# Kernel tuning notes

Measured on AMD Instinct MI355X. Metric: run time of the kernel, lower is better.

The kernel has to match this reference:

```python
import jax, jax.numpy as jnp
import numpy as np

M = 8      # number of modalities (len(ModalityType))
D = 256    # embedding_dim
B = 8192   # batch size


def setup_inputs() -> dict:
    key = jax.random.key(0)
    ks = jax.random.split(key, 12)
    s = 1.0 / np.sqrt(D)
    x = jax.random.normal(ks[0], (M, B, D), dtype=jnp.float32)
    reasoning_query = jax.random.normal(ks[1], (B, D), dtype=jnp.float32)
    # Per ordered modality pair (src, tgt): seq_len=1 MHA reduces to out_proj(V_proj(tgt)).
    Wv = jax.random.normal(ks[2], (M, M, D, D), dtype=jnp.float32) * s
    bv = jnp.zeros((M, M, D), dtype=jnp.float32)
    Wo = jax.random.normal(ks[3], (M, M, D, D), dtype=jnp.float32) * s
    bo = jnp.zeros((M, M, D), dtype=jnp.float32)
    # Per-modality fusion MLP: Linear(2D->D), ReLU, Linear(D->D)  (dropout = eval/identity)
    W1 = jax.random.normal(ks[4], (M, D, 2 * D), dtype=jnp.float32) * s
    b1 = jnp.zeros((M, D), dtype=jnp.float32)
    W2 = jax.random.normal(ks[5], (M, D, D), dtype=jnp.float32) * s
    b2 = jnp.zeros((M, D), dtype=jnp.float32)
    # Attention controller: Linear(2D->D), ReLU, Linear(D->1), Sigmoid
    Wc1 = jax.random.normal(ks[6], (D, 2 * D), dtype=jnp.float32) * s
    bc1 = jnp.zeros((D,), dtype=jnp.float32)
    wc2 = jax.random.normal(ks[7], (D,), dtype=jnp.float32) * s
    bc2 = jnp.zeros((1,), dtype=jnp.float32)
    return dict(x=x, reasoning_query=reasoning_query, Wv=Wv, bv=bv, Wo=Wo, bo=bo,
                W1=W1, b1=b1, W2=W2, b2=b2, Wc1=Wc1, bc1=bc1, wc2=wc2, bc2=bc2)


def reference(x, reasoning_query, Wv, bv, Wo, bo, W1, b1, W2, b2, Wc1, bc1, wc2, bc2):
    m = x.shape[0]
    # Cross-modal attention with seq_len=1: softmax over one key == 1, so the
    # attended output is exactly out_proj(V_proj(tgt_embedding)) for every pair.
    h = jnp.einsum('tbd,sted->stbe', x, Wv) + bv[:, :, None, :]          # [M,M,B,D]
    ctx = jnp.einsum('stbe,stoe->stbo', h, Wo) + bo[:, :, None, :]       # [M,M,B,D]
    # Mean over the M-1 target modalities (src != tgt), matching stack(...).mean(-1)
    offdiag = (1.0 - jnp.eye(m, dtype=x.dtype))[:, :, None, None]
    cross = (ctx * offdiag).sum(axis=1) / (m - 1)                         # [M,B,D]
    # Per-modality fusion MLP on cat([original, cross])
    comb = jnp.concatenate([x, cross], axis=-1)                           # [M,B,2D]
    hid = jax.nn.relu(jnp.einsum('mbf,mdf->mbd', comb, W1) + b1[:, None, :])
    fused = jnp.einsum('mbd,mod->mbo', hid, W2) + b2[:, None, :]          # [M,B,D]
    # Reasoning-query gating controller
    q = jnp.broadcast_to(reasoning_query[None], fused.shape)              # [M,B,D]
    qc = jnp.concatenate([q, fused], axis=-1)                             # [M,B,2D]
    ch = jax.nn.relu(jnp.einsum('mbf,df->mbd', qc, Wc1) + bc1)
    score = jax.nn.sigmoid(jnp.einsum('mbd,d->mb', ch, wc2) + bc2)        # [M,B]
    gated = fused * score[..., None]
    unified = gated.mean(axis=0)                                          # [B,D]
    return unified
```

## Files before the change

### kernel.cpp

```cpp
#include <hip/hip_runtime.h>

#define MMOD 8
#define BB 8192
#define DD 256

typedef unsigned short u16;
typedef __attribute__((ext_vector_type(8))) short s16x8;
typedef __attribute__((ext_vector_type(4))) float f32x4;
typedef __attribute__((ext_vector_type(8))) unsigned short u16x8;
typedef __attribute__((ext_vector_type(4))) unsigned short u16x4;
typedef __attribute__((ext_vector_type(4))) short s16x4;

typedef __attribute__((address_space(3))) unsigned short lds_u16;
typedef __attribute__((address_space(1))) const unsigned short gl_u16;

__device__ __forceinline__ float b2f(u16 u){ union{unsigned i; float f;} x; x.i=((unsigned)u)<<16; return x.f; }
__device__ __forceinline__ u16 f2b(float f){ union{float f; unsigned i;} x; x.f=f; unsigned r = x.i + 0x7FFF + ((x.i>>16)&1u); return (u16)(r>>16); }

__device__ __forceinline__ void async_cp16(const u16* g, u16* l){
  __builtin_amdgcn_global_load_lds((gl_u16*)g, (lds_u16*)l, 16, 0, 0);
}

struct ConvArgs {
  const float* src[10];
  u16*         dst[10];
  int          n[10];
};
__global__ void convert_kernel(ConvArgs a){
  const long long stride = (long long)gridDim.x * blockDim.x;
  const long long base   = (long long)blockIdx.x * blockDim.x + threadIdx.x;
  for (int s = 0; s < 10; s++){
    const int n  = a.n[s];
    const int n8 = n >> 3;
    const float* sp = a.src[s];
    u16* dst = a.dst[s];
    for (long long i = base; i < n8; i += stride){
      float4 lo = ((const float4*)sp)[i*2];
      float4 hi = ((const float4*)sp)[i*2+1];
      u16x8 p;
      p[0]=f2b(lo.x); p[1]=f2b(lo.y); p[2]=f2b(lo.z); p[3]=f2b(lo.w);
      p[4]=f2b(hi.x); p[5]=f2b(hi.y); p[6]=f2b(hi.z); p[7]=f2b(hi.w);
      *(u16x8*)(dst + (i<<3)) = p;
    }
    for (long long i = ((long long)n8<<3) + base; i < n; i += stride)
      dst[i] = f2b(sp[i]);
  }
}

__device__ __forceinline__ s16x8 load8_f32(const float* p, long long idx){
  float4 lo = *(const float4*)(p + idx);
  float4 hi = *(const float4*)(p + idx + 4);
  s16x8 r;
  r[0]=(short)f2b(lo.x); r[1]=(short)f2b(lo.y); r[2]=(short)f2b(lo.z); r[3]=(short)f2b(lo.w);
  r[4]=(short)f2b(hi.x); r[5]=(short)f2b(hi.y); r[6]=(short)f2b(hi.z); r[7]=(short)f2b(hi.w);
  return r;
}

struct GArgs {
  const u16* A;  long long a_z; long long a_piece; int lda;
  const u16* A2; long long a2_z;
  const u16* B;  long long b_z; int ldb;
  u16*       C;  long long c_z; long long c_npiece; int ldc;
  const u16* bias; long long bias_z;
  const float* cbias;
  const u16* addm;
  const u16* wc2;
  float*     scores;
  float scale;
  int K;
  int relu;
};

__global__ __launch_bounds__(512, 2) void gemm_8ph(GArgs g){
  alignas(16) __shared__ u16 L[65536];
  const int tid  = threadIdx.x;
  const int lane = tid & 63;
  const int w    = tid >> 6;
  const int z    = blockIdx.z;

  const int wr  = w >> 2;
  const int wcn = w & 3;
  const int fm  = lane & 15;
  const int fq  = lane >> 4;

  const long long arow0 = (long long)blockIdx.x * 256;
  const long long nrow0 = (long long)blockIdx.y * 256;

  const int r0  = tid >> 3;
  const int r1  = r0 + 64;
  const int cs  = tid & 7;
  const int gc0 = cs ^ (r0 & 7);
  const int gc1 = cs ^ (r1 & 7);
  const int ldst0 = (w * 64) * 8;
  const int ldst1 = (512 + w * 64) * 8;

  const u16* Az = g.A + (long long)z * g.a_z;
  const u16* Bz = g.B + (long long)z * g.b_z;

#define STAGE_A8(c, k0s, h) do{ \
    const u16* gb_ = Az + (long long)((k0s) >> 8) * g.a_piece + ((k0s) & 255); \
    const long long gr_ = arow0 + (h) * 128; \
    u16* lb_ = L + ((c) * 2 + 0) * 16384 + (h) * 8192; \
    async_cp16(gb_ + (gr_ + r0) * (long long)g.lda + gc0 * 8, lb_ + ldst0); \
    async_cp16(gb_ + (gr_ + r1) * (long long)g.lda + gc1 * 8, lb_ + ldst1); \
  }while(0)
#define STAGE_B8(c, k0s, h) do{ \
    const u16* gb_ = Bz + (k0s); \
    const long long gr_ = nrow0 + (h) * 128; \
    u16* lb_ = L + ((c) * 2 + 1) * 16384 + (h) * 8192; \
    async_cp16(gb_ + (gr_ + r0) * (long long)g.ldb + gc0 * 8, lb_ + ldst0); \
    async_cp16(gb_ + (gr_ + r1) * (long long)g.ldb + gc1 * 8, lb_ + ldst1); \
  }while(0)

  f32x4 acc[8][4];
  #pragma unroll
  for (int i=0;i<8;i++)
    #pragma unroll
    for (int j=0;j<4;j++)
      #pragma unroll
      for (int r=0;r<4;r++) acc[i][j][r] = 0.0f;

  const int T = g.K >> 6;

  STAGE_A8(0, 0, 0);  STAGE_A8(0, 0, 1);
  STAGE_B8(0, 0, 0);  STAGE_B8(0, 0, 1);
  STAGE_B8(1, 64, 0); STAGE_B8(1, 64, 1);
  asm volatile("s_waitcnt vmcnt(4)" ::: "memory");
  __builtin_amdgcn_s_barrier();

  int c = 0;
  for (int t = 0; t < T; ++t, c ^= 1){
    const int k0 = t << 6;
    const u16* lA = L + (c * 2 + 0) * 16384;
    const u16* lB = L + (c * 2 + 1) * 16384;
    s16x8 bf[4][2];
    #pragma unroll
    for (int q = 0; q < 4; ++q){
      if (q == 0 && t + 1 < T) STAGE_A8(c ^ 1, k0 + 64, 0);
      if (q == 1 && t + 1 < T) STAGE_A8(c ^ 1, k0 + 64, 1);
      if (q == 2 && t + 2 < T) STAGE_B8(c,     k0 + 128, 0);
      if (q == 3 && t + 2 < T) STAGE_B8(c,     k0 + 128, 1);
      if (q == 0){
        #pragma unroll
        for (int ni = 0; ni < 4; ni++){
          const int R = wcn * 64 + ni * 16 + fm;
          #pragma unroll
          for (int kk = 0; kk < 2; kk++){
            const int qf = kk * 4 + fq;
            bf[ni][kk] = *(const s16x8*)(lB + R * 64 + ((qf ^ (R & 7)) << 3));
          }
        }
      }
      s16x8 af[2][2];
      #pragma unroll
      for (int j = 0; j < 2; j++){
        const int R = wr * 128 + (q * 2 + j) * 16 + fm;
        #pragma unroll
        for (int kk = 0; kk < 2; kk++){
          const int qf = kk * 4 + fq;
          af[j][kk] = *(const s16x8*)(lA + R * 64 + ((qf ^ (R & 7)) << 3));
        }
      }
      __builtin_amdgcn_s_barrier();
      __builtin_amdgcn_s_setprio(1);
      #pragma unroll
      for (int kk = 0; kk < 2; kk++)
        #pragma unroll
        for (int j = 0; j < 2; j++)
          #pragma unroll
          for (int ni = 0; ni < 4; ni++)
            acc[q*2+j][ni] = __builtin_amdgcn_mfma_f32_16x16x32_bf16(af[j][kk], bf[ni][kk], acc[q*2+j][ni], 0, 0, 0);
      __builtin_amdgcn_s_setprio(0);
      if (q == 3){
        if (t + 2 < T)      asm volatile("s_waitcnt vmcnt(4)" ::: "memory");
        else if (t + 1 < T) asm volatile("s_waitcnt vmcnt(0)" ::: "memory");
      }
      __builtin_amdgcn_s_barrier();
    }
  }

  u16* Cb = g.C + (long long)z * g.c_z;
  const u16* biasp = g.bias ? g.bias + (long long)z * g.bias_z : (const u16*)0;
  #pragma unroll
  for (int mi = 0; mi < 8; mi++){
    #pragma unroll
    for (int ni = 0; ni < 4; ni++){
      const int n = (int)nrow0 + wcn * 64 + ni * 16 + fm;
      float bb = 0.0f;
      if (g.cbias) bb = g.cbias[n];
      else if (biasp) bb = b2f(biasp[n]);
      const long long cn = ((long long)(n >> 8)) * g.c_npiece + (n & 255);
      #pragma unroll
      for (int r = 0; r < 4; r++){
        const long long b = arow0 + wr * 128 + mi * 16 + fq * 4 + r;
        float v = acc[mi][ni][r] * g.scale + bb;
        if (g.relu) v = v > 0.0f ? v : 0.0f;
        Cb[cn + b * (long long)g.ldc] = f2b(v);
      }
    }
  }
#undef STAGE_A8
#undef STAGE_B8
}

__global__ __launch_bounds__(256, 4) void gemm_thin(GArgs g){
  alignas(16) __shared__ u16 lA[64*64];
  alignas(16) __shared__ u16 lB[256*64];
  const int tid  = threadIdx.x;
  const int lane = tid & 63;
  const int w    = tid >> 6;
  const int z    = blockIdx.z;

  const u16* Bbase = g.B + (long long)z * g.b_z;

  f32x4 acc[16];
  #pragma unroll
  for (int j=0;j<16;j++)
    #pragma unroll
    for (int r=0;r<4;r++) acc[j][r] = 0.0f;

  const int fm = lane & 15;
  const int fk = (lane >> 4) * 8;
  const long long arow0 = (long long)blockIdx.x * 64;

  const int sr = lane >> 3;
  const int sq = (lane & 7) ^ sr;

  for (int k0 = 0; k0 < g.K; k0 += 64){
    const u16* Abase0 = (g.A2 && k0 >= 256) ? (g.A2 + (long long)z * g.a2_z)
                                            : (g.A  + (long long)z * g.a_z);
    const u16* At = Abase0 + (long long)(k0 >> 8) * g.a_piece + (k0 & 255);
    const u16* Bt = Bbase + k0;
    __syncthreads();
    #pragma unroll
    for (int i=0;i<2;i++){
      int r = i*32 + w*8 + sr;
      async_cp16(At + (arow0 + r) * (long long)g.lda + sq*8, lA + (i*256 + w*64) * 8);
    }
    #pragma unroll
    for (int i=0;i<8;i++){
      int r = i*32 + w*8 + sr;
      async_cp16(Bt + (long long)r * g.ldb + sq*8, lB + (i*256 + w*64) * 8);
    }
    __syncthreads();
    #pragma unroll
    for (int kk = 0; kk < 64; kk += 32){
      const int qf = (kk + fk) >> 3;
      int ra = w*16 + fm;
      s16x8 af = *(const s16x8*)(lA + (ra*8 + (qf ^ (ra & 7))) * 8);
      #pragma unroll
      for (int ni=0; ni<16; ni++){
        int r = ni*16 + fm;
        s16x8 bfr = *(const s16x8*)(lB + (r*8 + (qf ^ (r & 7))) * 8);
        acc[ni] = __builtin_amdgcn_mfma_f32_16x16x32_bf16(af, bfr, acc[ni], 0, 0, 0);
      }
    }
  }

  u16* Cb = g.C + (long long)z * g.c_z;
  const u16* biasp = g.bias ? g.bias + (long long)z * g.bias_z : (const u16*)0;
  #pragma unroll
  for (int ni=0; ni<16; ni++){
    int n = ni*16 + fm;
    float bb = 0.0f;
    if (g.cbias) bb = g.cbias[n];
    else if (biasp) bb = b2f(biasp[n]);
    #pragma unroll
    for (int r=0; r<4; r++){
      long long b = arow0 + w*16 + (lane>>4)*4 + r;
      float v = acc[ni][r] * g.scale + bb;
      if (g.addm) v += b2f(g.addm[b*256 + n]);
      if (g.relu) v = v > 0.0f ? v : 0.0f;
      Cb[b * (long long)g.ldc + n] = f2b(v);
    }
  }
}

struct S34Args {
  const u16* X;
  const u16* CR;
  const u16* W1;
  const u16* W2;
  const u16* b1;
  const u16* b2;
  u16*       F;
};
__global__ __launch_bounds__(256, 2) void gemm_s34(S34Args a){
  alignas(16) __shared__ u16 lB[256*64];
  alignas(16) __shared__ u16 lH[64*256];
  u16* lA = lH;

  const int tid  = threadIdx.x;
  const int lane = tid & 63;
  const int w    = tid >> 6;
  const int z    = blockIdx.z;

  const int fm = lane & 15;
  const int fq = lane >> 4;
  const long long arow0 = (long long)blockIdx.x * 64;
  const long long BD = (long long)BB * DD;

  const int sr = lane >> 3;
  const int sq = (lane & 7) ^ sr;

  const u16* Xz  = a.X  + (long long)z * BD;
  const u16* CRz = a.CR + (long long)z * BD;
  const u16* W1z = a.W1 + (long long)z * 131072;
  const u16* W2z = a.W2 + (long long)z * 65536;

  f32x4 acc[16];
  #pragma unroll
  for (int j=0;j<16;j++)
    #pragma unroll
    for (int r=0;r<4;r++) acc[j][r] = 0.0f;

  for (int k0 = 0; k0 < 512; k0 += 64){
    const u16* At = (k0 < 256) ? (Xz + k0) : (CRz + (k0 - 256));
    const u16* Bt = W1z + k0;
    __syncthreads();
    #pragma unroll
    for (int i=0;i<2;i++){
      int r = i*32 + w*8 + sr;
      async_cp16(At + (arow0 + r) * 256 + sq*8, lA + (i*256 + w*64) * 8);
    }
    #pragma unroll
    for (int i=0;i<8;i++){
      int r = i*32 + w*8 + sr;
      async_cp16(Bt + (long long)r * 512 + sq*8, lB + (i*256 + w*64) * 8);
    }
    __syncthreads();
    #pragma unroll
    for (int kk = 0; kk < 64; kk += 32){
      const int qf = (kk >> 3) + fq;
      int ra = w*16 + fm;
      s16x8 af = *(const s16x8*)(lA + (ra*8 + (qf ^ (ra & 7))) * 8);
      #pragma unroll
      for (int ni=0; ni<16; ni++){
        int r = ni*16 + fm;
        s16x8 bfr = *(const s16x8*)(lB + (r*8 + (qf ^ (r & 7))) * 8);
        acc[ni] = __builtin_amdgcn_mfma_f32_16x16x32_bf16(bfr, af, acc[ni], 0, 0, 0);
      }
    }
  }

  __syncthreads();

  {
    const int b = w*16 + fm;
    #pragma unroll
    for (int ni=0; ni<16; ni++){
      s16x4 b1v = *(const s16x4*)(a.b1 + (long long)z*256 + ni*16 + fq*4);
      u16x4 pk;
      #pragma unroll
      for (int r=0; r<4; r++){
        float v = acc[ni][r] + b2f((u16)b1v[r]);
        v = v > 0.0f ? v : 0.0f;
        pk[r] = f2b(v);
      }
      const int c = ni*2 + (fq >> 1);
      const int csw = (c & ~7) | ((c & 7) ^ (b & 7));
      *(u16x4*)(lH + b*256 + csw*8 + (fq & 1)*4) = pk;
    }
  }

  f32x4 acc2[16];
  #pragma unroll
  for (int j=0;j<16;j++)
    #pragma unroll
    for (int r=0;r<4;r++) acc2[j][r] = 0.0f;

  for (int k0 = 0; k0 < 256; k0 += 64){
    const u16* Bt = W2z + k0;
    __syncthreads();
    #pragma unroll
    for (int i=0;i<8;i++){
      int r = i*32 + w*8 + sr;
      async_cp16(Bt + (long long)r * 256 + sq*8, lB + (i*256 + w*64) * 8);
    }
    __syncthreads();
    #pragma unroll
    for (int kk = 0; kk < 64; kk += 32){
      const int ra = w*16 + fm;
      const int qa = ((k0 + kk) >> 3) + fq;
      const int qsw = (qa & ~7) | ((qa & 7) ^ (ra & 7));
      s16x8 af = *(const s16x8*)(lH + ra*256 + qsw*8);
      const int qf = (kk >> 3) + fq;
      #pragma unroll
      for (int ni=0; ni<16; ni++){
        int r = ni*16 + fm;
        s16x8 bfr = *(const s16x8*)(lB + (r*8 + (qf ^ (r & 7))) * 8);
        acc2[ni] = __builtin_amdgcn_mfma_f32_16x16x32_bf16(af, bfr, acc2[ni], 0, 0, 0);
      }
    }
  }

  u16* Fz = a.F + (long long)z * BD;
  #pragma unroll
  for (int ni=0; ni<16; ni++){
    int o = ni*16 + fm;
    float bb = b2f(a.b2[(long long)z*256 + o]);
    #pragma unroll
    for (int r=0; r<4; r++){
      long long b = arow0 + w*16 + fq*4 + r;
      Fz[b * 256 + o] = f2b(acc2[ni][r] + bb);
    }
  }
}

__global__ __launch_bounds__(256, 4) void gemm_score(GArgs g){
  alignas(16) __shared__ u16 lA[64*64];
  alignas(16) __shared__ u16 lB[256*64];
  const int tid  = threadIdx.x;
  const int lane = tid & 63;
  const int w    = tid >> 6;
  const int z    = blockIdx.z;

  const u16* Bbase = g.B;

  f32x4 acc[16];
  #pragma unroll
  for (int j=0;j<16;j++)
    #pragma unroll
    for (int r=0;r<4;r++) acc[j][r] = 0.0f;

  const int fm = lane & 15;
  const int fk = (lane >> 4) * 8;
  const long long arow0 = (long long)blockIdx.x * 64;

  const int sr = lane >> 3;
  const int sq = (lane & 7) ^ sr;

  for (int k0 = 0; k0 < g.K; k0 += 64){
    const u16* At = g.A + (long long)z * g.a_z + k0;
    const u16* Bt = Bbase + k0;
    __syncthreads();
    #pragma unroll
    for (int i=0;i<2;i++){
      int r = i*32 + w*8 + sr;
      async_cp16(At + (arow0 + r) * (long long)g.lda + sq*8, lA + (i*256 + w*64) * 8);
    }
    #pragma unroll
    for (int i=0;i<8;i++){
      int r = i*32 + w*8 + sr;
      async_cp16(Bt + (long long)r * g.ldb + sq*8, lB + (i*256 + w*64) * 8);
    }
    __syncthreads();
    #pragma unroll
    for (int kk = 0; kk < 64; kk += 32){
      const int qf = (kk + fk) >> 3;
      int ra = w*16 + fm;
      s16x8 af = *(const s16x8*)(lA + (ra*8 + (qf ^ (ra & 7))) * 8);
      #pragma unroll
      for (int ni=0; ni<16; ni++){
        int r = ni*16 + fm;
        s16x8 bfr = *(const s16x8*)(lB + (r*8 + (qf ^ (r & 7))) * 8);
        acc[ni] = __builtin_amdgcn_mfma_f32_16x16x32_bf16(af, bfr, acc[ni], 0, 0, 0);
      }
    }
  }

  float p[4] = {0.f, 0.f, 0.f, 0.f};
  #pragma unroll
  for (int ni=0; ni<16; ni++){
    int n = ni*16 + fm;
    float bb = b2f(g.bias[n]);
    float wcv = b2f(g.wc2[n]);
    #pragma unroll
    for (int r=0; r<4; r++){
      long long b = arow0 + w*16 + (lane>>4)*4 + r;
      float v = acc[ni][r] + bb + b2f(g.addm[b*256 + n]);
      v = v > 0.0f ? v : 0.0f;
      p[r] += v * wcv;
    }
  }
  #pragma unroll
  for (int r=0; r<4; r++){
    #pragma unroll
    for (int off=1; off<16; off<<=1) p[r] += __shfl_xor(p[r], off);
  }
  if (fm == 0){
    float bc2f = g.cbias[0];
    #pragma unroll
    for (int r=0; r<4; r++){
      long long b = arow0 + w*16 + (lane>>4)*4 + r;
      g.scores[(long long)z*BB + b] = 1.0f / (1.0f + __expf(-(p[r] + bc2f)));
    }
  }
}

__global__ __launch_bounds__(256, 2) void build_wb(const float* Wo, const float* Wv, u16* WB){
  alignas(16) __shared__ u16 lA[128*64];
  alignas(16) __shared__ u16 lB[128*64];
  const int tid  = threadIdx.x;
  const int lane = tid & 63;
  const int w    = tid >> 6;
  const int z = blockIdx.z, s = z >> 3, t = z & 7;
  const long long zoff = (long long)z * 65536;

  f32x4 acc[4][4];
  #pragma unroll
  for (int i=0;i<4;i++)
    #pragma unroll
    for (int j=0;j<4;j++)
      #pragma unroll
      for (int r=0;r<4;r++) acc[i][j][r] = 0.0f;

  const int wr = (w >> 1) * 64, wc = (w & 1) * 64;
  const int fm = lane & 15;
  const int fk = (lane >> 4) * 8;

  int srow[4], sq[4];
  #pragma unroll
  for (int i=0;i<4;i++){
    int c = i*256 + tid;
    srow[i] = c >> 3;
    sq[i]   = (c & 7) ^ (srow[i] & 7);
  }

  for (int k0 = 0; k0 < 256; k0 += 64){
    s16x8 va[4], vt[4];
    #pragma unroll
    for (int i=0;i<4;i++){
      long long aidx = zoff + (long long)(blockIdx.x*128 + srow[i]) * 256 + k0 + sq[i]*8;
      va[i] = load8_f32(Wo, aidx);
    }
    #pragma unroll
    for (int j=0;j<4;j++){
      int id = j*256 + tid;
      int e  = id >> 4;
      int dc = (id & 15) * 8;
      long long bidx = zoff + (long long)(k0 + e) * 256 + blockIdx.y*128 + dc;
      vt[j] = load8_f32(Wv, bidx);
    }
    __syncthreads();
    #pragma unroll
    for (int i=0;i<4;i++){
      int c = i*256 + tid;
      *(s16x8*)(lA + c*8) = va[i];
    }
    #pragma unroll
    for (int j=0;j<4;j++){
      int id = j*256 + tid;
      int e  = id >> 4;
      int dc = (id & 15) * 8;
      #pragma unroll
      for (int u=0; u<8; u++){
        int d = dc + u;
        lB[(d*8 + ((e>>3) ^ (d & 7)))*8 + (e & 7)] = (u16)vt[j][u];
      }
    }
    __syncthreads();
    #pragma unroll
    for (int kk = 0; kk < 64; kk += 32){
      s16x8 af[4], bfr[4];
      const int qf = (kk + fk) >> 3;
      #pragma unroll
      for (int mi=0; mi<4; mi++){
        int r = wr + mi*16 + fm;
        af[mi] = *(const s16x8*)(lA + (r*8 + (qf ^ (r & 7))) * 8);
      }
      #pragma unroll
      for (int ni=0; ni<4; ni++){
        int r = wc + ni*16 + fm;
        bfr[ni] = *(const s16x8*)(lB + (r*8 + (qf ^ (r & 7))) * 8);
      }
      #pragma unroll
      for (int mi=0; mi<4; mi++)
        #pragma unroll
        for (int ni=0; ni<4; ni++)
          acc[mi][ni] = __builtin_amdgcn_mfma_f32_16x16x32_bf16(af[mi], bfr[ni], acc[mi][ni], 0, 0, 0);
    }
    __syncthreads();
  }
  const int diag = (s == t);
  #pragma unroll
  for (int mi=0; mi<4; mi++){
    #pragma unroll
    for (int ni=0; ni<4; ni++){
      int d = blockIdx.y*128 + wc + ni*16 + fm;
      #pragma unroll
      for (int r=0; r<4; r++){
        int o = blockIdx.x*128 + wr + mi*16 + (lane>>4)*4 + r;
        float v = diag ? 0.0f : acc[mi][ni][r];
        WB[(long long)(s*256 + o) * 2048 + t*256 + d] = f2b(v);
      }
    }
  }
}

__global__ __launch_bounds__(256) void cb_kernel(const float* bv, const float* Wo, const float* bo, float* cb){
  int z = blockIdx.x, s = z >> 3, t = z & 7;
  if (s == t) return;
  int lane = threadIdx.x & 63, w = threadIdx.x >> 6;
  float4 bvv = *(const float4*)(bv + (long long)z*256 + lane*4);
  #pragma unroll
  for (int i=0; i<16; i++){
    int row = blockIdx.y*64 + w*16 + i;
    float4 wv4 = *(const float4*)(Wo + (long long)z*65536 + (long long)row*256 + lane*4);
    float p = wv4.x*bvv.x + wv4.y*bvv.y + wv4.z*bvv.z + wv4.w*bvv.w;
    #pragma unroll
    for (int off=32; off>0; off>>=1) p += __shfl_xor(p, off);
    if (lane == 0)
      atomicAdd(&cb[s*256 + row], (p + bo[(long long)z*256 + row]) * (1.0f/7.0f));
  }
}

__global__ __launch_bounds__(256) void final_gate(const u16* fused, const float* scores, float* out){
  int b = blockIdx.x;
  int tid = threadIdx.x;
  float sc[8];
  #pragma unroll
  for (int m=0; m<8; m++) sc[m] = scores[(long long)m*BB + b];
  float acc = 0.0f;
  #pragma unroll
  for (int m=0; m<8; m++)
    acc += b2f(fused[((long long)m*BB + b)*256 + tid]) * sc[m];
  out[(long long)b*256 + tid] = acc * 0.125f;
}

extern "C" void kernel_launch(void* const* d_in, const int* in_sizes, int n_in,
                              void* d_out, int out_size, void* d_ws, size_t ws_size,
                              hipStream_t stream){
  const float* x   = (const float*)d_in[0];
  const float* q   = (const float*)d_in[1];
  const float* Wv  = (const float*)d_in[2];
  const float* bv  = (const float*)d_in[3];
  const float* Wo  = (const float*)d_in[4];
  const float* bo  = (const float*)d_in[5];
  const float* W1  = (const float*)d_in[6];
  const float* b1  = (const float*)d_in[7];
  const float* W2  = (const float*)d_in[8];
  const float* b2  = (const float*)d_in[9];
  const float* Wc1 = (const float*)d_in[10];
  const float* bc1 = (const float*)d_in[11];
  const float* wc2 = (const float*)d_in[12];
  const float* bc2 = (const float*)d_in[13];

  char* ws = (char*)d_ws;
  u16*   xb    = (u16*)(ws + 0LL);
  u16*   qb    = (u16*)(ws + 33554432LL);
  u16*   cross = (u16*)(ws + 37748736LL);
  u16*   WB    = (u16*)(ws + 104857600LL);
  u16*   W1b   = (u16*)(ws + 113246208LL);
  u16*   W2b   = (u16*)(ws + 115343360LL);
  u16*   Wc1b  = (u16*)(ws + 116391936LL);
  u16*   b1b   = (u16*)(ws + 116654080LL);
  u16*   b2b   = (u16*)(ws + 116658176LL);
  u16*   bc1b  = (u16*)(ws + 116662272LL);
  u16*   wc2b  = (u16*)(ws + 116662784LL);
  float* bc2f  = (float*)(ws + 116663296LL);
  float* cb    = (float*)(ws + 116663424LL);
  u16*   fused = xb;
  u16*   qctx  = WB;
  float* scores = (float*)(ws + 104857600LL + 4194304LL);

  ConvArgs ca{};
  ca.src[0]=x;   ca.dst[0]=xb;   ca.n[0]=MMOD*BB*DD;
  ca.src[1]=q;   ca.dst[1]=qb;   ca.n[1]=BB*DD;
  ca.src[2]=W1;  ca.dst[2]=W1b;  ca.n[2]=MMOD*DD*2*DD;
  ca.src[3]=W2;  ca.dst[3]=W2b;  ca.n[3]=MMOD*DD*DD;
  ca.src[4]=Wc1; ca.dst[4]=Wc1b; ca.n[4]=DD*2*DD;
  ca.src[5]=b1;  ca.dst[5]=b1b;  ca.n[5]=MMOD*DD;
  ca.src[6]=b2;  ca.dst[6]=b2b;  ca.n[6]=MMOD*DD;
  ca.src[7]=bc1; ca.dst[7]=bc1b; ca.n[7]=DD;
  ca.src[8]=wc2; ca.dst[8]=wc2b; ca.n[8]=DD;
  ca.src[9]=bc2; ca.dst[9]=bc1b; ca.n[9]=0;
  convert_kernel<<<1024, 256, 0, stream>>>(ca);
  hipMemcpyAsync(bc2f, bc2, sizeof(float), hipMemcpyDeviceToDevice, stream);

  hipMemsetAsync(cb, 0, 2048*sizeof(float), stream);
  build_wb<<<dim3(2,2,64), 256, 0, stream>>>(Wo, Wv, WB);
  cb_kernel<<<dim3(64,4), 256, 0, stream>>>(bv, Wo, bo, cb);

  const long long BD = (long long)BB * DD;

  GArgs g2{};
  g2.A = xb; g2.a_z = 0; g2.a_piece = BD; g2.lda = 256; g2.A2 = 0; g2.a2_z = 0;
  g2.B = WB; g2.b_z = 0; g2.ldb = 2048;
  g2.C = cross; g2.c_z = 0; g2.c_npiece = BD; g2.ldc = 256;
  g2.bias = 0; g2.bias_z = 0; g2.cbias = cb; g2.addm = 0; g2.wc2 = 0; g2.scores = 0;
  g2.scale = 1.0f/7.0f; g2.K = 2048; g2.relu = 0;
  gemm_8ph<<<dim3(32,8,1), 512, 0, stream>>>(g2);

  GArgs g5a{};
  g5a.A = qb; g5a.a_z = 0; g5a.a_piece = 0; g5a.lda = 256; g5a.A2 = 0; g5a.a2_z = 0;
  g5a.B = Wc1b; g5a.b_z = 0; g5a.ldb = 512;
  g5a.C = qctx; g5a.c_z = 0; g5a.c_npiece = 0; g5a.ldc = 256;
  g5a.bias = 0; g5a.bias_z = 0; g5a.cbias = 0; g5a.addm = 0; g5a.wc2 = 0; g5a.scores = 0;
  g5a.scale = 1.0f; g5a.K = 256; g5a.relu = 0;
  gemm_thin<<<dim3(128,1,1), 256, 0, stream>>>(g5a);

  S34Args s34{};
  s34.X = xb; s34.CR = cross; s34.W1 = W1b; s34.W2 = W2b;
  s34.b1 = b1b; s34.b2 = b2b; s34.F = fused;
  gemm_s34<<<dim3(128,1,8), 256, 0, stream>>>(s34);

  GArgs g5b{};
  g5b.A = fused; g5b.a_z = BD; g5b.a_piece = 0; g5b.lda = 256; g5b.A2 = 0; g5b.a2_z = 0;
  g5b.B = Wc1b + 256; g5b.b_z = 0; g5b.ldb = 512;
  g5b.C = 0; g5b.c_z = 0; g5b.c_npiece = 0; g5b.ldc = 0;
  g5b.bias = bc1b; g5b.bias_z = 0; g5b.cbias = bc2f; g5b.addm = qctx;
  g5b.wc2 = wc2b; g5b.scores = scores;
  g5b.scale = 1.0f; g5b.K = 256; g5b.relu = 1;
  gemm_score<<<dim3(128,1,8), 256, 0, stream>>>(g5b);

  final_gate<<<dim3(BB), 256, 0, stream>>>(fused, scores, (float*)d_out);

  (void)in_sizes; (void)n_in; (void)out_size; (void)ws_size;
}
```

Measured before the change: 349.6 us.

## Fuse gating score GEMM into fusion MLP kernel, reusing fused tile from LDS

Merges the gemm_score kernel into the fusion-MLP kernel, which becomes gemm_s345. The fused output tile stays in LDS in swizzled form and feeds directly into the controller GEMM, so it is no longer re-read from global memory, and one launch is removed. The second MFMA swaps its operand order so each lane holds a contiguous column chunk for vectorized stores to both global and LDS. This adds a third GEMM phase to the kernel, which raises register pressure and may lower occupancy.

```diff
diff --git a/kernel.cpp b/kernel.cpp
--- a/kernel.cpp
+++ b/kernel.cpp
@@ -63,9 +63,6 @@
   u16*       C;  long long c_z; long long c_npiece; int ldc;
   const u16* bias; long long bias_z;
   const float* cbias;
-  const u16* addm;
-  const u16* wc2;
-  float*     scores;
   float scale;
   int K;
   int relu;
@@ -269,7 +266,6 @@
     for (int r=0; r<4; r++){
       long long b = arow0 + w*16 + (lane>>4)*4 + r;
       float v = acc[ni][r] * g.scale + bb;
-      if (g.addm) v += b2f(g.addm[b*256 + n]);
       if (g.relu) v = v > 0.0f ? v : 0.0f;
       Cb[b * (long long)g.ldc + n] = f2b(v);
     }
@@ -281,11 +277,17 @@
   const u16* CR;
   const u16* W1;
   const u16* W2;
+  const u16* Wc1h;
   const u16* b1;
   const u16* b2;
+  const u16* bc1;
+  const u16* wc2;
+  const u16* qctx;
+  const float* bc2f;
+  float*     scores;
   u16*       F;
 };
-__global__ __launch_bounds__(256, 2) void gemm_s34(S34Args a){
+__global__ __launch_bounds__(256, 2) void gemm_s345(S34Args a){
   alignas(16) __shared__ u16 lB[256*64];
   alignas(16) __shared__ u16 lH[64*256];
   u16* lA = lH;
@@ -389,72 +391,57 @@
       for (int ni=0; ni<16; ni++){
         int r = ni*16 + fm;
         s16x8 bfr = *(const s16x8*)(lB + (r*8 + (qf ^ (r & 7))) * 8);
-        acc2[ni] = __builtin_amdgcn_mfma_f32_16x16x32_bf16(af, bfr, acc2[ni], 0, 0, 0);
-      }
-    }
-  }
-
-  u16* Fz = a.F + (long long)z * BD;
-  #pragma unroll
-  for (int ni=0; ni<16; ni++){
-    int o = ni*16 + fm;
-    float bb = b2f(a.b2[(long long)z*256 + o]);
-    #pragma unroll
-    for (int r=0; r<4; r++){
-      long long b = arow0 + w*16 + fq*4 + r;
-      Fz[b * 256 + o] = f2b(acc2[ni][r] + bb);
-    }
-  }
-}
-
-__global__ __launch_bounds__(256, 4) void gemm_score(GArgs g){
-  alignas(16) __shared__ u16 lA[64*64];
-  alignas(16) __shared__ u16 lB[256*64];
-  const int tid  = threadIdx.x;
-  const int lane = tid & 63;
-  const int w    = tid >> 6;
-  const int z    = blockIdx.z;
-
-  const u16* Bbase = g.B;
-
-  f32x4 acc[16];
+        acc2[ni] = __builtin_amdgcn_mfma_f32_16x16x32_bf16(bfr, af, acc2[ni], 0, 0, 0);
+      }
+    }
+  }
+
+  __syncthreads();
+
+  {
+    const int b = w*16 + fm;
+    u16* Fz = a.F + (long long)z * BD;
+    #pragma unroll
+    for (int ni=0; ni<16; ni++){
+      s16x4 b2v = *(const s16x4*)(a.b2 + (long long)z*256 + ni*16 + fq*4);
+      u16x4 pk;
+      #pragma unroll
+      for (int r=0; r<4; r++)
+        pk[r] = f2b(acc2[ni][r] + b2f((u16)b2v[r]));
+      *(u16x4*)(Fz + (arow0 + b)*256 + ni*16 + fq*4) = pk;
+      const int c = ni*2 + (fq >> 1);
+      const int csw = (c & ~7) | ((c & 7) ^ (b & 7));
+      *(u16x4*)(lH + b*256 + csw*8 + (fq & 1)*4) = pk;
+    }
+  }
+
+  f32x4 acc3[16];
   #pragma unroll
   for (int j=0;j<16;j++)
     #pragma unroll
-    for (int r=0;r<4;r++) acc[j][r] = 0.0f;
-
-  const int fm = lane & 15;
-  const int fk = (lane >> 4) * 8;
-  const long long arow0 = (long long)blockIdx.x * 64;
-
-  const int sr = lane >> 3;
-  const int sq = (lane & 7) ^ sr;
-
-  for (int k0 = 0; k0 < g.K; k0 += 64){
-    const u16* At = g.A + (long long)z * g.a_z + k0;
-    const u16* Bt = Bbase + k0;
-    __syncthreads();
-    #pragma unroll
-    for (int i=0;i<2;i++){
-      int r = i*32 + w*8 + sr;
-      async_cp16(At + (arow0 + r) * (long long)g.lda + sq*8, lA + (i*256 + w*64) * 8);
-    }
+    for (int r=0;r<4;r++) acc3[j][r] = 0.0f;
+
+  for (int k0 = 0; k0 < 256; k0 += 64){
+    const u16* Bt = a.Wc1h + k0;
+    __syncthreads();
     #pragma unroll
     for (int i=0;i<8;i++){
       int r = i*32 + w*8 + sr;
-      async_cp16(Bt + (long long)r * g.ldb + sq*8, lB + (i*256 + w*64) * 8);
+      async_cp16(Bt + (long long)r * 512 + sq*8, lB + (i*256 + w*64) * 8);
     }
     __syncthreads();
     #pragma unroll
     for (int kk = 0; kk < 64; kk += 32){
-      const int qf = (kk + fk) >> 3;
-      int ra = w*16 + fm;
-      s16x8 af = *(const s16x8*)(lA + (ra*8 + (qf ^ (ra & 7))) * 8);
+      const int ra = w*16 + fm;
+      const int qa = ((k0 + kk) >> 3) + fq;
+      const int qsw = (qa & ~7) | ((qa & 7) ^ (ra & 7));
+      s16x8 af = *(const s16x8*)(lH + ra*256 + qsw*8);
+      const int qf = (kk >> 3) + fq;
       #pragma unroll
       for (int ni=0; ni<16; ni++){
         int r = ni*16 + fm;
         s16x8 bfr = *(const s16x8*)(lB + (r*8 + (qf ^ (r & 7))) * 8);
-        acc[ni] = __builtin_amdgcn_mfma_f32_16x16x32_bf16(af, bfr, acc[ni], 0, 0, 0);
+        acc3[ni] = __builtin_amdgcn_mfma_f32_16x16x32_bf16(af, bfr, acc3[ni], 0, 0, 0);
       }
     }
   }
@@ -463,12 +450,12 @@
   #pragma unroll
   for (int ni=0; ni<16; ni++){
     int n = ni*16 + fm;
-    float bb = b2f(g.bias[n]);
-    float wcv = b2f(g.wc2[n]);
+    float bb = b2f(a.bc1[n]);
+    float wcv = b2f(a.wc2[n]);
     #pragma unroll
     for (int r=0; r<4; r++){
-      long long b = arow0 + w*16 + (lane>>4)*4 + r;
-      float v = acc[ni][r] + bb + b2f(g.addm[b*256 + n]);
+      long long b = arow0 + w*16 + fq*4 + r;
+      float v = acc3[ni][r] + bb + b2f(a.qctx[b*256 + n]);
       v = v > 0.0f ? v : 0.0f;
       p[r] += v * wcv;
     }
@@ -479,11 +466,11 @@
     for (int off=1; off<16; off<<=1) p[r] += __shfl_xor(p[r], off);
   }
   if (fm == 0){
-    float bc2f = g.cbias[0];
+    float bc2v = a.bc2f[0];
     #pragma unroll
     for (int r=0; r<4; r++){
-      long long b = arow0 + w*16 + (lane>>4)*4 + r;
-      g.scores[(long long)z*BB + b] = 1.0f / (1.0f + __expf(-(p[r] + bc2f)));
+      long long b = arow0 + w*16 + fq*4 + r;
+      a.scores[(long long)z*BB + b] = 1.0f / (1.0f + __expf(-(p[r] + bc2v)));
     }
   }
 }
@@ -678,7 +665,7 @@
   g2.A = xb; g2.a_z = 0; g2.a_piece = BD; g2.lda = 256; g2.A2 = 0; g2.a2_z = 0;
   g2.B = WB; g2.b_z = 0; g2.ldb = 2048;
   g2.C = cross; g2.c_z = 0; g2.c_npiece = BD; g2.ldc = 256;
-  g2.bias = 0; g2.bias_z = 0; g2.cbias = cb; g2.addm = 0; g2.wc2 = 0; g2.scores = 0;
+  g2.bias = 0; g2.bias_z = 0; g2.cbias = cb;
   g2.scale = 1.0f/7.0f; g2.K = 2048; g2.relu = 0;
   gemm_8ph<<<dim3(32,8,1), 512, 0, stream>>>(g2);
 
@@ -686,23 +673,15 @@
   g5a.A = qb; g5a.a_z = 0; g5a.a_piece = 0; g5a.lda = 256; g5a.A2 = 0; g5a.a2_z = 0;
   g5a.B = Wc1b; g5a.b_z = 0; g5a.ldb = 512;
   g5a.C = qctx; g5a.c_z = 0; g5a.c_npiece = 0; g5a.ldc = 256;
-  g5a.bias = 0; g5a.bias_z = 0; g5a.cbias = 0; g5a.addm = 0; g5a.wc2 = 0; g5a.scores = 0;
+  g5a.bias = 0; g5a.bias_z = 0; g5a.cbias = 0;
   g5a.scale = 1.0f; g5a.K = 256; g5a.relu = 0;
   gemm_thin<<<dim3(128,1,1), 256, 0, stream>>>(g5a);
 
   S34Args s34{};
-  s34.X = xb; s34.CR = cross; s34.W1 = W1b; s34.W2 = W2b;
-  s34.b1 = b1b; s34.b2 = b2b; s34.F = fused;
-  gemm_s34<<<dim3(128,1,8), 256, 0, stream>>>(s34);
-
-  GArgs g5b{};
-  g5b.A = fused; g5b.a_z = BD; g5b.a_piece = 0; g5b.lda = 256; g5b.A2 = 0; g5b.a2_z = 0;
-  g5b.B = Wc1b + 256; g5b.b_z = 0; g5b.ldb = 512;
-  g5b.C = 0; g5b.c_z = 0; g5b.c_npiece = 0; g5b.ldc = 0;
-  g5b.bias = bc1b; g5b.bias_z = 0; g5b.cbias = bc2f; g5b.addm = qctx;
-  g5b.wc2 = wc2b; g5b.scores = scores;
-  g5b.scale = 1.0f; g5b.K = 256; g5b.relu = 1;
-  gemm_score<<<dim3(128,1,8), 256, 0, stream>>>(g5b);
+  s34.X = xb; s34.CR = cross; s34.W1 = W1b; s34.W2 = W2b; s34.Wc1h = Wc1b + 256;
+  s34.b1 = b1b; s34.b2 = b2b; s34.bc1 = bc1b; s34.wc2 = wc2b;
+  s34.qctx = qctx; s34.bc2f = bc2f; s34.scores = scores; s34.F = fused;
+  gemm_s345<<<dim3(128,1,8), 256, 0, stream>>>(s34);
 
   final_gate<<<dim3(BB), 256, 0, stream>>>(fused, scores, (float*)d_out);
 
```

New measurement: 337.9 us. -3.3%, faster.
